# Optimization experiments

Hardware: AMD Instinct MI355X
Metric: run time of the kernel (lower is better)

## Reference

```python
import jax, jax.numpy as jnp
import numpy as np

S, H = 8192, 7168          # tokens, hidden
D0, D1 = 1536, 576         # q_a_proj dim, kv_a_proj_with_mqa dim (output_offset = [0, 1536, 2112])
R = 64                     # LoRA rank per slice


def setup_inputs() -> dict:
    key = jax.random.key(0)
    k1, k2, k3, k4, k5 = jax.random.split(key, 5)
    x = jax.random.normal(k1, (S, H), dtype=jnp.float32)
    W = jax.random.normal(k2, (D0 + D1, H), dtype=jnp.float32) * 0.02
    bias = jax.random.normal(k3, (D0 + D1,), dtype=jnp.float32) * 0.02
    # stacked LoRA-A for both slices: [n_slices*r, hidden]
    A_buffer = jax.random.normal(k4, (2 * R, H), dtype=jnp.float32) * 0.02
    # LoRA-B padded to max slice dim: [n_slices, max_out_dim, r]; only first D1 rows of slice 1 are valid
    B_buffer = jax.random.normal(k5, (2, D0, R), dtype=jnp.float32) * 0.02
    return {"x": x, "W": W, "bias": bias, "A_buffer": A_buffer, "B_buffer": B_buffer}


def reference(x, W, bias, A_buffer, B_buffer):
    # base replicated linear: [S, D0+D1]
    out = jnp.einsum('sh,oh->so', x, W) + bias
    # fused LoRA-A for both slices: [S, 2*R]
    la = jnp.einsum('sh,rh->sr', x, A_buffer)
    # segmented LoRA-B (run_qkv_lora with n_slices=2): scatter-add into offset slices
    out = out.at[:, :D0].add(jnp.einsum('sr,or->so', la[:, :R], B_buffer[0, :D0]))
    out = out.at[:, D0:].add(jnp.einsum('sr,or->so', la[:, R:], B_buffer[1, :D1]))
    return out
```

## Files before the change

kernel.cpp:

```cpp
#include <hip/hip_runtime.h>
#include <hip/hip_bf16.h>

#define S_DIM 8192
#define H_DIM 7168
#define D0_DIM 1536
#define D1_DIM 576
#define N_DIM 2112
#define R_DIM 64
#define LA_WIDTH 128

#define K_EXT 7296
#define NT32 228
#define N_PAD 2176
#define KSPLIT 8
#define KCHUNK 896

#define XE_RB 512
#define WE_RB 136

typedef __attribute__((ext_vector_type(4))) float f32x4;
typedef __attribute__((ext_vector_type(8))) short bf16x8;
typedef __attribute__((ext_vector_type(4))) short bf16x4;

__device__ __forceinline__ short f2bf(float f) {
    union { __hip_bfloat16 h; short s; } u;
    u.h = __float2bfloat16(f);
    return u.s;
}

__device__ __forceinline__ bf16x8 pack8(f32x4 a, f32x4 b) {
    bf16x8 r;
    r[0] = f2bf(a[0]); r[1] = f2bf(a[1]); r[2] = f2bf(a[2]); r[3] = f2bf(a[3]);
    r[4] = f2bf(b[0]); r[5] = f2bf(b[1]); r[6] = f2bf(b[2]); r[7] = f2bf(b[3]);
    return r;
}

__device__ __forceinline__ void gload_lds16(const short* g, short* l) {
    __builtin_amdgcn_global_load_lds(
        (const __attribute__((address_space(1))) unsigned int*)(const void*)g,
        (__attribute__((address_space(3))) unsigned int*)(void*)l, 16, 0, 0);
}

__global__ __launch_bounds__(256)
void convert_w(const float* __restrict__ W, short* __restrict__ we) {
    unsigned id = blockIdx.x * 256u + threadIdx.x;
    unsigned rb  = id / 14336u;
    unsigned rem = id % 14336u;
    unsigned kb  = rem >> 6, sl = rem & 63u;
    unsigned r16 = sl >> 2;
    unsigned c   = (sl & 3u) ^ (((r16 >> 3) & 1u) << 1);
    unsigned row = rb * 16u + r16;
    unsigned k   = kb * 32u + c * 8u;
    const float* p = W + (size_t)row * H_DIM + k;
    f32x4 a = *(const f32x4*)p;
    f32x4 b = *(const f32x4*)(p + 4);
    *(bf16x8*)(we + ((size_t)rb * NT32 + kb) * 512u + sl * 8u) = pack8(a, b);
}

__global__ __launch_bounds__(256)
void convert_w_lora(const float* __restrict__ Bbuf, short* __restrict__ we) {
    unsigned id = blockIdx.x * 256u + threadIdx.x;
    unsigned rb  = id >> 8;
    unsigned rem = id & 255u;
    unsigned kb4 = rem >> 6, sl = rem & 63u;
    unsigned r16 = sl >> 2;
    unsigned c   = (sl & 3u) ^ (((r16 >> 3) & 1u) << 1);
    unsigned row = rb * 16u + r16;
    unsigned k   = kb4 * 32u + c * 8u;
    bf16x8 v = {};
    if (row < N_DIM) {
        const bool s1 = row >= D0_DIM;
        const unsigned lo = s1 ? 64u : 0u;
        if (k >= lo && k < lo + 64u) {
            const float* p = Bbuf + ((size_t)(s1 ? 1u : 0u) * D0_DIM +
                                     (row - (s1 ? D0_DIM : 0u))) * R_DIM + (k - lo);
            f32x4 a = *(const f32x4*)p;
            f32x4 b = *(const f32x4*)(p + 4);
            v = pack8(a, b);
        }
    }
    *(bf16x8*)(we + ((size_t)rb * NT32 + (224u + kb4)) * 512u + sl * 8u) = v;
}

__global__ __launch_bounds__(256, 2)
void lora_a_pass(const float* __restrict__ x, const float* __restrict__ A,
                 float* __restrict__ part, short* __restrict__ xe) {
    __shared__ __align__(16) short sX[128 * 40];
    __shared__ __align__(16) short sA[128 * 40];

    const int tid = threadIdx.x;
    const int m0 = blockIdx.x * 128;
    const int k0 = blockIdx.y * KCHUNK;
    const int wave = tid >> 6, lane = tid & 63;
    const int wm = (wave & 1) * 64, wn = (wave >> 1) * 64;
    const int fr = lane & 15, fq = lane >> 4;

    f32x4 acc[4][4] = {};

    const int srow = tid >> 1, shalf = (tid & 1) * 16;
    const float* xP = x + (size_t)(m0 + srow) * H_DIM + k0 + shalf;
    const float* aP = A + (size_t)srow * H_DIM + k0 + shalf;

    const unsigned rbx = (unsigned)(m0 + srow) >> 4;
    const unsigned r16 = (unsigned)srow & 15u;
    const unsigned kb0 = (unsigned)k0 >> 5;
    const unsigned c0  = (unsigned)shalf >> 3;
    const unsigned sx  = ((r16 >> 3) & 1u) << 1;
    const unsigned sl0 = r16 * 4u + (c0 ^ sx);
    const unsigned sl1 = r16 * 4u + ((c0 + 1u) ^ sx);
    short* xeB = xe + ((size_t)rbx * NT32 + kb0) * 512u;

    short* sXw = sX + srow * 40 + shalf;
    short* sAw = sA + srow * 40 + shalf;
    const short* sXr = sX + (wm + fr) * 40 + fq * 8;
    const short* sAr = sA + (wn + fr) * 40 + fq * 8;

    for (int it = 0; it < KCHUNK / 32; ++it) {
        const float* px = xP + it * 32;
        const float* pa = aP + it * 32;
        f32x4 x0 = *(const f32x4*)(px);
        f32x4 x1 = *(const f32x4*)(px + 4);
        f32x4 x2 = *(const f32x4*)(px + 8);
        f32x4 x3 = *(const f32x4*)(px + 12);
        f32x4 a0 = *(const f32x4*)(pa);
        f32x4 a1 = *(const f32x4*)(pa + 4);
        f32x4 a2 = *(const f32x4*)(pa + 8);
        f32x4 a3 = *(const f32x4*)(pa + 12);
        bf16x8 px0 = pack8(x0, x1), px1 = pack8(x2, x3);
        bf16x8 pa0 = pack8(a0, a1), pa1 = pack8(a2, a3);

        *(bf16x8*)(xeB + (size_t)it * 512 + sl0 * 8u) = px0;
        *(bf16x8*)(xeB + (size_t)it * 512 + sl1 * 8u) = px1;

        __syncthreads();
        *(bf16x8*)(sXw) = px0; *(bf16x8*)(sXw + 8) = px1;
        *(bf16x8*)(sAw) = pa0; *(bf16x8*)(sAw + 8) = pa1;
        __syncthreads();

        bf16x8 af[4], bfg[4];
#pragma unroll
        for (int i = 0; i < 4; ++i) af[i] = *(const bf16x8*)(sXr + i * 16 * 40);
#pragma unroll
        for (int i = 0; i < 4; ++i) bfg[i] = *(const bf16x8*)(sAr + i * 16 * 40);
#pragma unroll
        for (int mi = 0; mi < 4; ++mi)
#pragma unroll
            for (int ni = 0; ni < 4; ++ni)
                acc[mi][ni] = __builtin_amdgcn_mfma_f32_16x16x32_bf16(
                    af[mi], bfg[ni], acc[mi][ni], 0, 0, 0);
    }

    float* pBase = part + (size_t)blockIdx.y * S_DIM * LA_WIDTH;
#pragma unroll
    for (int ni = 0; ni < 4; ++ni) {
        const int col = wn + ni * 16 + fr;
#pragma unroll
        for (int mi = 0; mi < 4; ++mi) {
            const int row = m0 + wm + mi * 16 + fq * 4;
#pragma unroll
            for (int r = 0; r < 4; ++r)
                pBase[(size_t)(row + r) * LA_WIDTH + col] = acc[mi][ni][r];
        }
    }
}

__global__ __launch_bounds__(256)
void lora_reduce(const float* __restrict__ part, short* __restrict__ xe) {
    unsigned id = blockIdx.x * 256u + threadIdx.x;
    unsigned row = id >> 4, c8 = (id & 15u) * 8u;
    f32x4 s0 = {}, s1 = {};
#pragma unroll
    for (int kz = 0; kz < KSPLIT; ++kz) {
        const float* p = part + ((size_t)kz * S_DIM + row) * LA_WIDTH + c8;
        s0 += *(const f32x4*)(p);
        s1 += *(const f32x4*)(p + 4);
    }
    unsigned rbx = row >> 4, r16 = row & 15u;
    unsigned kb = 224u + (c8 >> 5);
    unsigned cc = (c8 >> 3) & 3u;
    unsigned sl = r16 * 4u + (cc ^ (((r16 >> 3) & 1u) << 1));
    *(bf16x8*)(xe + ((size_t)rbx * NT32 + kb) * 512u + sl * 8u) = pack8(s0, s1);
}

__global__ __launch_bounds__(256, 2)
void main_gemm_tiled(const short* __restrict__ xe, const short* __restrict__ we,
                     const float* __restrict__ bias, float* __restrict__ out) {
    __shared__ __align__(16) short lds[3 * 12288];

    const int tid = threadIdx.x;
    const int bx = blockIdx.x;
    const int xcd = bx & 7, p = bx >> 3;
    const int tile = xcd * 68 + p;
    const int m0 = (tile / 17) * 256;
    const int n0 = (tile % 17) * 128;

    const int wave = tid >> 6, lane = tid & 63;
    const int wm = (wave & 1) * 128;
    const int wn = (wave >> 1) * 64;
    const int fr = lane & 15, fq = lane >> 4;

    f32x4 acc[8][4] = {};

    const short* gp[6];
    int ldoff[6];
    {
        const short* xe_pan = xe + (size_t)(m0 >> 4) * NT32 * 512 + lane * 8;
        const short* we_pan = we + (size_t)(n0 >> 4) * NT32 * 512 + lane * 8;
#pragma unroll
        for (int i = 0; i < 6; ++i) {
            const int idx = wave * 6 + i;
            if (idx < 16) { gp[i] = xe_pan + (size_t)idx * NT32 * 512; ldoff[i] = idx * 512; }
            else          { gp[i] = we_pan + (size_t)(idx - 16) * NT32 * 512; ldoff[i] = 8192 + (idx - 16) * 512; }
        }
    }

    const int swz  = (fq ^ ((fr >> 3) << 1)) * 8;
    const int aoff = (wm + fr) * 32 + swz;
    const int boff = 8192 + (wn + fr) * 32 + swz;

#pragma unroll
    for (int i = 0; i < 6; ++i) gload_lds16(gp[i], lds + ldoff[i]);
#pragma unroll
    for (int i = 0; i < 6; ++i) gload_lds16(gp[i] + 512, lds + 12288 + ldoff[i]);

    for (int t = 0; t < NT32; t += 3) {
#pragma unroll
        for (int b = 0; b < 3; ++b) {
            const int kt = t + b;
            asm volatile("s_waitcnt vmcnt(6)" ::: "memory");
            __builtin_amdgcn_s_barrier();
            __builtin_amdgcn_sched_barrier(0);
            int tt = kt + 2; if (tt >= NT32) tt -= NT32;
            const int db = (b + 2) % 3;
#pragma unroll
            for (int i = 0; i < 6; ++i)
                gload_lds16(gp[i] + (size_t)tt * 512, lds + db * 12288 + ldoff[i]);
            __builtin_amdgcn_sched_barrier(0);
            const short* pa = lds + b * 12288 + aoff;
            const short* pb = lds + b * 12288 + boff;
            bf16x8 af[8], brf[4];
#pragma unroll
            for (int m = 0; m < 8; ++m) af[m] = *(const bf16x8*)(pa + m * 512);
#pragma unroll
            for (int n = 0; n < 4; ++n) brf[n] = *(const bf16x8*)(pb + n * 512);
            __builtin_amdgcn_s_setprio(1);
#pragma unroll
            for (int m = 0; m < 8; ++m)
#pragma unroll
                for (int n = 0; n < 4; ++n)
                    acc[m][n] = __builtin_amdgcn_mfma_f32_16x16x32_bf16(
                        af[m], brf[n], acc[m][n], 0, 0, 0);
            __builtin_amdgcn_s_setprio(0);
            __builtin_amdgcn_sched_barrier(0);
        }
    }
    asm volatile("s_waitcnt vmcnt(0)" ::: "memory");

#pragma unroll
    for (int n = 0; n < 4; ++n) {
        const int col = n0 + wn + n * 16 + fr;
        if (col < N_DIM) {
            const float bv = bias[col];
#pragma unroll
            for (int m = 0; m < 8; ++m) {
                const int row = m0 + wm + m * 16 + fq * 4;
#pragma unroll
                for (int r = 0; r < 4; ++r)
                    out[(size_t)(row + r) * N_DIM + col] = acc[m][n][r] + bv;
            }
        }
    }
}

__global__ __launch_bounds__(256, 2)
void lora_a_gemm(const float* __restrict__ x, const float* __restrict__ Abuf,
                 float* __restrict__ la) {
    __shared__ __align__(16) short sX[32 * 40];
    __shared__ __align__(16) short sA[128 * 40];
    const int tid = threadIdx.x;
    const int m0 = blockIdx.x * 32;
    const int wave = tid >> 6, lane = tid & 63;
    const int fr = lane & 15, fq = lane >> 4;
    const int wn = wave * 32;
    f32x4 acc[2][2] = {};
    const int xrow = tid >> 3, xcol = (tid & 7) * 4;
    const float* xP = x + (size_t)(m0 + xrow) * H_DIM + xcol;
    short* sXw = sX + xrow * 40 + xcol;
    const int arow = tid >> 1, ahalf = (tid & 1) * 16;
    const float* aP = Abuf + (size_t)arow * H_DIM + ahalf;
    short* sAw = sA + arow * 40 + ahalf;
    const short* sXr = sX + fr * 40 + fq * 8;
    const short* sAr = sA + (wn + fr) * 40 + fq * 8;
    for (int kt = 0; kt < H_DIM / 32; ++kt) {
        f32x4 xv = *(const f32x4*)(xP + kt * 32);
        f32x4 a0 = *(const f32x4*)(aP + kt * 32);
        f32x4 a1 = *(const f32x4*)(aP + kt * 32 + 4);
        f32x4 a2 = *(const f32x4*)(aP + kt * 32 + 8);
        f32x4 a3 = *(const f32x4*)(aP + kt * 32 + 12);
        bf16x4 xs;
        xs[0] = f2bf(xv[0]); xs[1] = f2bf(xv[1]);
        xs[2] = f2bf(xv[2]); xs[3] = f2bf(xv[3]);
        bf16x8 as0 = pack8(a0, a1), as1 = pack8(a2, a3);
        __syncthreads();
        *(bf16x4*)(sXw) = xs;
        *(bf16x8*)(sAw) = as0;
        *(bf16x8*)(sAw + 8) = as1;
        __syncthreads();
        bf16x8 xf0 = *(const bf16x8*)(sXr);
        bf16x8 xf1 = *(const bf16x8*)(sXr + 16 * 40);
        bf16x8 af0 = *(const bf16x8*)(sAr);
        bf16x8 af1 = *(const bf16x8*)(sAr + 16 * 40);
        acc[0][0] = __builtin_amdgcn_mfma_f32_16x16x32_bf16(xf0, af0, acc[0][0], 0, 0, 0);
        acc[0][1] = __builtin_amdgcn_mfma_f32_16x16x32_bf16(xf0, af1, acc[0][1], 0, 0, 0);
        acc[1][0] = __builtin_amdgcn_mfma_f32_16x16x32_bf16(xf1, af0, acc[1][0], 0, 0, 0);
        acc[1][1] = __builtin_amdgcn_mfma_f32_16x16x32_bf16(xf1, af1, acc[1][1], 0, 0, 0);
    }
#pragma unroll
    for (int ni = 0; ni < 2; ++ni) {
        const int col = wn + ni * 16 + fr;
#pragma unroll
        for (int mi = 0; mi < 2; ++mi) {
            const int row = m0 + mi * 16 + fq * 4;
#pragma unroll
            for (int r = 0; r < 4; ++r)
                la[(size_t)(row + r) * LA_WIDTH + col] = acc[mi][ni][r];
        }
    }
}

#define LDS_STRIDE 40
__global__ __launch_bounds__(256, 2)
void main_gemm(const float* __restrict__ x, const float* __restrict__ W,
               const float* __restrict__ bias, const float* __restrict__ Bbuf,
               const float* __restrict__ la, float* __restrict__ out) {
    __shared__ __align__(16) short sA[128 * LDS_STRIDE];
    __shared__ __align__(16) short sB[128 * LDS_STRIDE];
    const int tid = threadIdx.x;
    const int n0 = blockIdx.x * 128, m0 = blockIdx.y * 128;
    const int wave = tid >> 6, lane = tid & 63;
    const int wm = (wave & 1) * 64, wn = (wave >> 1) * 64;
    const int fr = lane & 15, fq = lane >> 4;
    f32x4 acc[4][4] = {};
    const int srow = tid >> 1, shalf = (tid & 1) * 16;
    const float* xP = x + (size_t)(m0 + srow) * H_DIM + shalf;
    const int wRow = n0 + srow;
    const bool wValid = wRow < N_DIM;
    const float* wP = W + (size_t)wRow * H_DIM + shalf;
    const int slice = (n0 >= D0_DIM) ? 1 : 0;
    const int oCol = wRow - slice * D0_DIM;
    const bool bValid = wValid && (oCol < (slice ? D1_DIM : D0_DIM));
    const float* laP = la + (size_t)(m0 + srow) * LA_WIDTH + slice * R_DIM + shalf;
    const float* bP = Bbuf + ((size_t)slice * D0_DIM + oCol) * R_DIM + shalf;
    short* sAw = sA + srow * LDS_STRIDE + shalf;
    short* sBw = sB + srow * LDS_STRIDE + shalf;
    const short* sAr = sA + (wm + fr) * LDS_STRIDE + fq * 8;
    const short* sBr = sB + (wn + fr) * LDS_STRIDE + fq * 8;
    const int KT = H_DIM / 32;
    for (int it = 0; it < KT + 2; ++it) {
        const float *pa, *pb;
        bool vb;
        if (it < KT) { pa = xP + it * 32; pb = wP + it * 32; vb = wValid; }
        else { const int lt = it - KT; pa = laP + lt * 32; pb = bP + lt * 32; vb = bValid; }
        f32x4 a0 = *(const f32x4*)(pa);
        f32x4 a1 = *(const f32x4*)(pa + 4);
        f32x4 a2 = *(const f32x4*)(pa + 8);
        f32x4 a3 = *(const f32x4*)(pa + 12);
        f32x4 z = {0.f, 0.f, 0.f, 0.f};
        f32x4 b0 = z, b1 = z, b2 = z, b3 = z;
        if (vb) {
            b0 = *(const f32x4*)(pb); b1 = *(const f32x4*)(pb + 4);
            b2 = *(const f32x4*)(pb + 8); b3 = *(const f32x4*)(pb + 12);
        }
        bf16x8 pa0 = pack8(a0, a1), pa1 = pack8(a2, a3);
        bf16x8 pb0 = pack8(b0, b1), pb1 = pack8(b2, b3);
        __syncthreads();
        *(bf16x8*)(sAw) = pa0; *(bf16x8*)(sAw + 8) = pa1;
        *(bf16x8*)(sBw) = pb0; *(bf16x8*)(sBw + 8) = pb1;
        __syncthreads();
        bf16x8 af[4], bfg[4];
#pragma unroll
        for (int i = 0; i < 4; ++i) af[i] = *(const bf16x8*)(sAr + i * 16 * LDS_STRIDE);
#pragma unroll
        for (int i = 0; i < 4; ++i) bfg[i] = *(const bf16x8*)(sBr + i * 16 * LDS_STRIDE);
#pragma unroll
        for (int mi = 0; mi < 4; ++mi)
#pragma unroll
            for (int ni = 0; ni < 4; ++ni)
                acc[mi][ni] = __builtin_amdgcn_mfma_f32_16x16x32_bf16(
                    af[mi], bfg[ni], acc[mi][ni], 0, 0, 0);
    }
#pragma unroll
    for (int ni = 0; ni < 4; ++ni) {
        const int col = n0 + wn + ni * 16 + fr;
        if (col < N_DIM) {
            const float bv = bias[col];
#pragma unroll
            for (int mi = 0; mi < 4; ++mi) {
                const int row = m0 + wm + mi * 16 + fq * 4;
#pragma unroll
                for (int r = 0; r < 4; ++r)
                    out[(size_t)(row + r) * N_DIM + col] = acc[mi][ni][r] + bv;
            }
        }
    }
}

extern "C" void kernel_launch(void* const* d_in, const int* in_sizes, int n_in,
                              void* d_out, int out_size, void* d_ws, size_t ws_size,
                              hipStream_t stream) {
    const float* x    = (const float*)d_in[0];
    const float* W    = (const float*)d_in[1];
    const float* bias = (const float*)d_in[2];
    const float* A    = (const float*)d_in[3];
    const float* B    = (const float*)d_in[4];
    float* out = (float*)d_out;

    const size_t xe_bytes   = (size_t)XE_RB * NT32 * 1024;
    const size_t we_bytes   = (size_t)WE_RB * NT32 * 1024;
    const size_t part_bytes = (size_t)KSPLIT * S_DIM * LA_WIDTH * 4;
    const size_t tail = (we_bytes > part_bytes) ? we_bytes : part_bytes;

    if (ws_size >= xe_bytes + tail) {
        short* xe = (short*)d_ws;
        short* we = (short*)((char*)d_ws + xe_bytes);
        float* part = (float*)((char*)d_ws + xe_bytes);

        lora_a_pass<<<dim3(S_DIM / 128, KSPLIT), dim3(256), 0, stream>>>(x, A, part, xe);
        lora_reduce<<<dim3(S_DIM * 16 / 256), dim3(256), 0, stream>>>(part, xe);
        convert_w<<<dim3(132 * 224 * 64 / 256), dim3(256), 0, stream>>>(W, we);
        convert_w_lora<<<dim3(WE_RB * 4 * 64 / 256), dim3(256), 0, stream>>>(B, we);
        main_gemm_tiled<<<dim3(32 * 17), dim3(256), 0, stream>>>(xe, we, bias, out);
    } else {
        float* la = (float*)d_ws;
        lora_a_gemm<<<dim3(S_DIM / 32), dim3(256), 0, stream>>>(x, A, la);
        main_gemm<<<dim3(N_DIM / 128 + 1, S_DIM / 128), dim3(256), 0, stream>>>(
            x, W, bias, B, la, out);
    }
}
```

Measured before the change: 689.1 us.

## Fuse weight conversion with LoRA-A pass, atomically reduce into output scratch

Merges the W and LoRA-B bf16 conversion kernels into the LoRA-A split-K kernel as extra blocks in one launch, so conversion and the LoRA-A GEMM run concurrently. The per-split partial buffer and its reduction are replaced by atomicAdd into a zeroed scratch region placed in the output buffer, which is read back into the extended x operand before the main GEMM overwrites it. The LoRA-A loop also gains register prefetch of the next K slice and double-buffered LDS with a single barrier per iteration. The cost is float atomics, an extra memset, and nondeterministic summation order.

```diff
diff --git a/kernel.cpp b/kernel.cpp
--- a/kernel.cpp
+++ b/kernel.cpp
@@ -18,6 +18,9 @@
 #define XE_RB 512
 #define WE_RB 136
 
+#define CONV_BLKS 256
+#define CONV_ITEMS (WE_RB * NT32 * 64)
+
 typedef __attribute__((ext_vector_type(4))) float f32x4;
 typedef __attribute__((ext_vector_type(8))) short bf16x8;
 typedef __attribute__((ext_vector_type(4))) short bf16x4;
@@ -41,56 +44,57 @@
         (__attribute__((address_space(3))) unsigned int*)(void*)l, 16, 0, 0);
 }
 
-__global__ __launch_bounds__(256)
-void convert_w(const float* __restrict__ W, short* __restrict__ we) {
-    unsigned id = blockIdx.x * 256u + threadIdx.x;
-    unsigned rb  = id / 14336u;
-    unsigned rem = id % 14336u;
-    unsigned kb  = rem >> 6, sl = rem & 63u;
-    unsigned r16 = sl >> 2;
-    unsigned c   = (sl & 3u) ^ (((r16 >> 3) & 1u) << 1);
-    unsigned row = rb * 16u + r16;
-    unsigned k   = kb * 32u + c * 8u;
-    const float* p = W + (size_t)row * H_DIM + k;
-    f32x4 a = *(const f32x4*)p;
-    f32x4 b = *(const f32x4*)(p + 4);
-    *(bf16x8*)(we + ((size_t)rb * NT32 + kb) * 512u + sl * 8u) = pack8(a, b);
-}
-
-__global__ __launch_bounds__(256)
-void convert_w_lora(const float* __restrict__ Bbuf, short* __restrict__ we) {
-    unsigned id = blockIdx.x * 256u + threadIdx.x;
-    unsigned rb  = id >> 8;
-    unsigned rem = id & 255u;
-    unsigned kb4 = rem >> 6, sl = rem & 63u;
-    unsigned r16 = sl >> 2;
-    unsigned c   = (sl & 3u) ^ (((r16 >> 3) & 1u) << 1);
-    unsigned row = rb * 16u + r16;
-    unsigned k   = kb4 * 32u + c * 8u;
-    bf16x8 v = {};
-    if (row < N_DIM) {
-        const bool s1 = row >= D0_DIM;
-        const unsigned lo = s1 ? 64u : 0u;
-        if (k >= lo && k < lo + 64u) {
-            const float* p = Bbuf + ((size_t)(s1 ? 1u : 0u) * D0_DIM +
-                                     (row - (s1 ? D0_DIM : 0u))) * R_DIM + (k - lo);
-            f32x4 a = *(const f32x4*)p;
-            f32x4 b = *(const f32x4*)(p + 4);
-            v = pack8(a, b);
-        }
-    }
-    *(bf16x8*)(we + ((size_t)rb * NT32 + (224u + kb4)) * 512u + sl * 8u) = v;
-}
-
 __global__ __launch_bounds__(256, 2)
-void lora_a_pass(const float* __restrict__ x, const float* __restrict__ A,
-                 float* __restrict__ part, short* __restrict__ xe) {
-    __shared__ __align__(16) short sX[128 * 40];
-    __shared__ __align__(16) short sA[128 * 40];
-
+void fused_stage1(const float* __restrict__ x, const float* __restrict__ W,
+                  const float* __restrict__ A, const float* __restrict__ Bbuf,
+                  float* __restrict__ la, short* __restrict__ xe,
+                  short* __restrict__ we) {
+    if (blockIdx.x < CONV_BLKS) {
+        const unsigned base0 = blockIdx.x * 256u + threadIdx.x;
+#pragma unroll 1
+        for (int itr = 0; itr < 31; ++itr) {
+            unsigned id = base0 + (unsigned)itr * (CONV_BLKS * 256u);
+            if (id < CONV_ITEMS) {
+                unsigned rb  = id / 14592u;
+                unsigned rem = id % 14592u;
+                unsigned kb  = rem >> 6, sl = rem & 63u;
+                unsigned r16 = sl >> 2;
+                unsigned c   = (sl & 3u) ^ (((r16 >> 3) & 1u) << 1);
+                unsigned row = rb * 16u + r16;
+                bf16x8 v = {};
+                if (row < N_DIM) {
+                    if (kb < 224u) {
+                        unsigned k = kb * 32u + c * 8u;
+                        const float* p = W + (size_t)row * H_DIM + k;
+                        f32x4 a = *(const f32x4*)p;
+                        f32x4 b = *(const f32x4*)(p + 4);
+                        v = pack8(a, b);
+                    } else {
+                        unsigned kl = (kb - 224u) * 32u + c * 8u;
+                        const bool s1 = row >= D0_DIM;
+                        const unsigned lo = s1 ? 64u : 0u;
+                        if (kl >= lo && kl < lo + 64u) {
+                            const float* p = Bbuf + ((size_t)(s1 ? 1u : 0u) * D0_DIM +
+                                                     (row - (s1 ? D0_DIM : 0u))) * R_DIM + (kl - lo);
+                            f32x4 a = *(const f32x4*)p;
+                            f32x4 b = *(const f32x4*)(p + 4);
+                            v = pack8(a, b);
+                        }
+                    }
+                }
+                *(bf16x8*)(we + ((size_t)rb * NT32 + kb) * 512u + sl * 8u) = v;
+            }
+        }
+        return;
+    }
+
+    __shared__ __align__(16) short sX[2][128 * 40];
+    __shared__ __align__(16) short sA[2][128 * 40];
+
+    const int bx = blockIdx.x - CONV_BLKS;
     const int tid = threadIdx.x;
-    const int m0 = blockIdx.x * 128;
-    const int k0 = blockIdx.y * KCHUNK;
+    const int m0 = (bx >> 3) * 128;
+    const int k0 = (bx & 7) * KCHUNK;
     const int wave = tid >> 6, lane = tid & 63;
     const int wm = (wave & 1) * 64, wn = (wave >> 1) * 64;
     const int fr = lane & 15, fq = lane >> 4;
@@ -110,47 +114,66 @@
     const unsigned sl1 = r16 * 4u + ((c0 + 1u) ^ sx);
     short* xeB = xe + ((size_t)rbx * NT32 + kb0) * 512u;
 
-    short* sXw = sX + srow * 40 + shalf;
-    short* sAw = sA + srow * 40 + shalf;
-    const short* sXr = sX + (wm + fr) * 40 + fq * 8;
-    const short* sAr = sA + (wn + fr) * 40 + fq * 8;
-
+    const int swoff = srow * 40 + shalf;
+    const int xr_off = (wm + fr) * 40 + fq * 8;
+    const int ar_off = (wn + fr) * 40 + fq * 8;
+
+    f32x4 cx0 = *(const f32x4*)(xP);
+    f32x4 cx1 = *(const f32x4*)(xP + 4);
+    f32x4 cx2 = *(const f32x4*)(xP + 8);
+    f32x4 cx3 = *(const f32x4*)(xP + 12);
+    f32x4 ca0 = *(const f32x4*)(aP);
+    f32x4 ca1 = *(const f32x4*)(aP + 4);
+    f32x4 ca2 = *(const f32x4*)(aP + 8);
+    f32x4 ca3 = *(const f32x4*)(aP + 12);
+    f32x4 nx0 = {}, nx1 = {}, nx2 = {}, nx3 = {};
+    f32x4 na0 = {}, na1 = {}, na2 = {}, na3 = {};
+
+#pragma unroll 1
     for (int it = 0; it < KCHUNK / 32; ++it) {
-        const float* px = xP + it * 32;
-        const float* pa = aP + it * 32;
-        f32x4 x0 = *(const f32x4*)(px);
-        f32x4 x1 = *(const f32x4*)(px + 4);
-        f32x4 x2 = *(const f32x4*)(px + 8);
-        f32x4 x3 = *(const f32x4*)(px + 12);
-        f32x4 a0 = *(const f32x4*)(pa);
-        f32x4 a1 = *(const f32x4*)(pa + 4);
-        f32x4 a2 = *(const f32x4*)(pa + 8);
-        f32x4 a3 = *(const f32x4*)(pa + 12);
-        bf16x8 px0 = pack8(x0, x1), px1 = pack8(x2, x3);
-        bf16x8 pa0 = pack8(a0, a1), pa1 = pack8(a2, a3);
+        if (it < KCHUNK / 32 - 1) {
+            const float* px = xP + (it + 1) * 32;
+            const float* pa = aP + (it + 1) * 32;
+            nx0 = *(const f32x4*)(px);
+            nx1 = *(const f32x4*)(px + 4);
+            nx2 = *(const f32x4*)(px + 8);
+            nx3 = *(const f32x4*)(px + 12);
+            na0 = *(const f32x4*)(pa);
+            na1 = *(const f32x4*)(pa + 4);
+            na2 = *(const f32x4*)(pa + 8);
+            na3 = *(const f32x4*)(pa + 12);
+        }
+        bf16x8 px0 = pack8(cx0, cx1), px1 = pack8(cx2, cx3);
+        bf16x8 pa0 = pack8(ca0, ca1), pa1 = pack8(ca2, ca3);
 
         *(bf16x8*)(xeB + (size_t)it * 512 + sl0 * 8u) = px0;
         *(bf16x8*)(xeB + (size_t)it * 512 + sl1 * 8u) = px1;
 
-        __syncthreads();
-        *(bf16x8*)(sXw) = px0; *(bf16x8*)(sXw + 8) = px1;
-        *(bf16x8*)(sAw) = pa0; *(bf16x8*)(sAw + 8) = pa1;
-        __syncthreads();
+        short* bX = &sX[it & 1][0];
+        short* bA = &sA[it & 1][0];
+        *(bf16x8*)(bX + swoff) = px0; *(bf16x8*)(bX + swoff + 8) = px1;
+        *(bf16x8*)(bA + swoff) = pa0; *(bf16x8*)(bA + swoff + 8) = pa1;
+
+        asm volatile("s_waitcnt lgkmcnt(0)" ::: "memory");
+        __builtin_amdgcn_s_barrier();
+        __builtin_amdgcn_sched_barrier(0);
 
         bf16x8 af[4], bfg[4];
 #pragma unroll
-        for (int i = 0; i < 4; ++i) af[i] = *(const bf16x8*)(sXr + i * 16 * 40);
-#pragma unroll
-        for (int i = 0; i < 4; ++i) bfg[i] = *(const bf16x8*)(sAr + i * 16 * 40);
+        for (int i = 0; i < 4; ++i) af[i] = *(const bf16x8*)(bX + xr_off + i * 640);
+#pragma unroll
+        for (int i = 0; i < 4; ++i) bfg[i] = *(const bf16x8*)(bA + ar_off + i * 640);
 #pragma unroll
         for (int mi = 0; mi < 4; ++mi)
 #pragma unroll
             for (int ni = 0; ni < 4; ++ni)
                 acc[mi][ni] = __builtin_amdgcn_mfma_f32_16x16x32_bf16(
                     af[mi], bfg[ni], acc[mi][ni], 0, 0, 0);
-    }
-
-    float* pBase = part + (size_t)blockIdx.y * S_DIM * LA_WIDTH;
+
+        cx0 = nx0; cx1 = nx1; cx2 = nx2; cx3 = nx3;
+        ca0 = na0; ca1 = na1; ca2 = na2; ca3 = na3;
+    }
+
 #pragma unroll
     for (int ni = 0; ni < 4; ++ni) {
         const int col = wn + ni * 16 + fr;
@@ -159,22 +182,18 @@
             const int row = m0 + wm + mi * 16 + fq * 4;
 #pragma unroll
             for (int r = 0; r < 4; ++r)
-                pBase[(size_t)(row + r) * LA_WIDTH + col] = acc[mi][ni][r];
+                atomicAdd(&la[(size_t)(row + r) * LA_WIDTH + col], acc[mi][ni][r]);
         }
     }
 }
 
 __global__ __launch_bounds__(256)
-void lora_reduce(const float* __restrict__ part, short* __restrict__ xe) {
+void la_to_xe(const float* __restrict__ la, short* __restrict__ xe) {
     unsigned id = blockIdx.x * 256u + threadIdx.x;
     unsigned row = id >> 4, c8 = (id & 15u) * 8u;
-    f32x4 s0 = {}, s1 = {};
-#pragma unroll
-    for (int kz = 0; kz < KSPLIT; ++kz) {
-        const float* p = part + ((size_t)kz * S_DIM + row) * LA_WIDTH + c8;
-        s0 += *(const f32x4*)(p);
-        s1 += *(const f32x4*)(p + 4);
-    }
+    const float* p = la + (size_t)row * LA_WIDTH + c8;
+    f32x4 s0 = *(const f32x4*)(p);
+    f32x4 s1 = *(const f32x4*)(p + 4);
     unsigned rbx = row >> 4, r16 = row & 15u;
     unsigned kb = 224u + (c8 >> 5);
     unsigned cc = (c8 >> 3) & 3u;
@@ -415,20 +434,19 @@
     const float* B    = (const float*)d_in[4];
     float* out = (float*)d_out;
 
-    const size_t xe_bytes   = (size_t)XE_RB * NT32 * 1024;
-    const size_t we_bytes   = (size_t)WE_RB * NT32 * 1024;
-    const size_t part_bytes = (size_t)KSPLIT * S_DIM * LA_WIDTH * 4;
-    const size_t tail = (we_bytes > part_bytes) ? we_bytes : part_bytes;
-
-    if (ws_size >= xe_bytes + tail) {
+    const size_t xe_bytes = (size_t)XE_RB * NT32 * 1024;
+    const size_t we_bytes = (size_t)WE_RB * NT32 * 1024;
+    const size_t la_bytes = (size_t)S_DIM * LA_WIDTH * 4;
+
+    if (ws_size >= xe_bytes + we_bytes) {
         short* xe = (short*)d_ws;
         short* we = (short*)((char*)d_ws + xe_bytes);
-        float* part = (float*)((char*)d_ws + xe_bytes);
-
-        lora_a_pass<<<dim3(S_DIM / 128, KSPLIT), dim3(256), 0, stream>>>(x, A, part, xe);
-        lora_reduce<<<dim3(S_DIM * 16 / 256), dim3(256), 0, stream>>>(part, xe);
-        convert_w<<<dim3(132 * 224 * 64 / 256), dim3(256), 0, stream>>>(W, we);
-        convert_w_lora<<<dim3(WE_RB * 4 * 64 / 256), dim3(256), 0, stream>>>(B, we);
+        float* la = (float*)d_out;
+
+        hipMemsetAsync(d_out, 0, la_bytes, stream);
+        fused_stage1<<<dim3(CONV_BLKS + 512), dim3(256), 0, stream>>>(
+            x, W, A, B, la, xe, we);
+        la_to_xe<<<dim3(S_DIM * 16 / 256), dim3(256), 0, stream>>>(la, xe);
         main_gemm_tiled<<<dim3(32 * 17), dim3(256), 0, stream>>>(xe, we, bias, out);
     } else {
         float* la = (float*)d_ws;
```

Result: no change. 686.7 us (-0.3%).
